# Kernel optimization log

Measured on AMD Instinct MI355X. Metric: run time of the kernel, lower is better.

## Reference

```python
import jax, jax.numpy as jnp
import numpy as np


def setup_inputs() -> dict:
    key = jax.random.key(0)
    k1, k2, k3 = jax.random.split(key, 3)
    B, C, D, S = 16, 80, 1024, 14  # batch, num_classes, feature dim, conv size
    return {
        "batch_size": B,
        "img_feature_map": jax.random.normal(k1, (B, D, S, S), dtype=jnp.float32),
        "word_features": jax.random.normal(k2, (C, D), dtype=jnp.float32),
        "fc_a_w": jax.random.normal(k3, (D,), dtype=jnp.float32) / np.float32(np.sqrt(D)),
        "fc_a_b": jnp.zeros((), dtype=jnp.float32),
    }


def reference(batch_size, img_feature_map, word_features, fc_a_w, fc_a_b):
    # img_feature_map: [B, D, H, W] -> [B, H, W, D]
    img = jnp.transpose(img_feature_map, (0, 2, 3, 1))
    # class-wise gated feature: tanh(img * word) -> [B, H, W, C, D]
    gated = jnp.tanh(img[:, :, :, None, :] * word_features[None, None, None, :, :])
    # rank-1 linear score: [B, H, W, C]
    scores = jnp.einsum('bhwcd,d->bhwc', gated, fc_a_w) + fc_a_b
    B, H, W, C = scores.shape
    # softmax over spatial positions (H*W) per (batch, class)
    coef = jax.nn.softmax(scores.reshape(B, H * W, C), axis=1).reshape(B, H, W, C)
    # attention-weighted spatial pooling -> [B, C, D]
    return jnp.einsum('bhwc,bhwd->bcd', coef, img)
```

## Files before the change

kernel.cpp:

```cpp
#include <hip/hip_runtime.h>

#define BB 16
#define CC 80
#define DD 1024
#define HW 196
#define NSP (BB * HW)
#define NCH 8
#define DCH 128
#define CPB 4
#define NCQ (CC / CPB)
#define PCL 16
#define TWO_LOG2E 2.8853900817779268f

__global__ __launch_bounds__(256) void scores_k(const float* __restrict__ img,
                                                const float* __restrict__ word,
                                                const float* __restrict__ fa,
                                                float* __restrict__ partial) {
    const int g = blockIdx.x * 256 + threadIdx.x;
    if (g >= NSP) return;
    const int b  = g / HW;
    const int hw = g - b * HW;
    const int d0 = blockIdx.y * DCH;
    const int c0 = blockIdx.z * CPB;

    const float* ip = img + ((size_t)b * DD + d0) * HW + hw;

    float p[CPB];
#pragma unroll
    for (int k = 0; k < CPB; ++k) p[k] = 0.f;

    for (int q = 0; q < DCH / 32; ++q) {
        float iv[32];
        const float* qp = ip + (size_t)q * 32 * HW;
#pragma unroll
        for (int i = 0; i < 32; ++i)
            iv[i] = qp[(size_t)i * HW] * TWO_LOG2E;

        const float* fp = fa + d0 + q * 32;
#pragma unroll
        for (int k = 0; k < CPB; ++k) {
            const float* wp = word + (size_t)(c0 + k) * DD + d0 + q * 32;
            float p0 = 0.f, p1 = 0.f;
#pragma unroll
            for (int i = 0; i < 32; i += 2) {
                float y0 = iv[i]     * wp[i];
                float y1 = iv[i + 1] * wp[i + 1];
                float e0 = __builtin_amdgcn_exp2f(y0);
                float e1 = __builtin_amdgcn_exp2f(y1);
                float r0 = __builtin_amdgcn_rcpf(e0 + 1.f);
                float r1 = __builtin_amdgcn_rcpf(e1 + 1.f);
                p0 = fmaf(fp[i],     r0, p0);
                p1 = fmaf(fp[i + 1], r1, p1);
            }
            p[k] += p0 + p1;
        }
    }

#pragma unroll
    for (int k = 0; k < CPB; ++k)
        partial[(((size_t)b * NCH + blockIdx.y) * CC + (c0 + k)) * HW + hw]
            = (-TWO_LOG2E) * p[k];
}

__global__ __launch_bounds__(256) void poolmax_k(const float* __restrict__ img,
                                                 const float* __restrict__ partial,
                                                 float* __restrict__ out) {
    __shared__ float it[64 * HW];
    __shared__ float ct[PCL * HW];
    const int b  = blockIdx.x;
    const int d0 = blockIdx.y * 64;
    const int cg = blockIdx.z * PCL;
    const int t  = threadIdx.x;
    const int w  = t >> 6, l = t & 63;

    const float4* src = (const float4*)(img + ((size_t)b * DD + d0) * HW);
    float4* dst = (float4*)it;
    for (int j = t; j < 64 * HW / 4; j += 256) dst[j] = src[j];

#pragma unroll
    for (int r = 4 * w; r < 4 * w + 4; ++r) {
        const int c = cg + r;
        float x0 = 0.f, x1 = 0.f, x2 = 0.f, x3 = 0.f;
#pragma unroll
        for (int ch = 0; ch < NCH; ++ch) {
            const float* pp = partial + (((size_t)b * NCH + ch) * CC + c) * HW;
            x0 += pp[l];
            x1 += pp[l + 64];
            x2 += pp[l + 128];
            if (l < HW - 192) x3 += pp[l + 192];
        }
        float x3m = (l < HW - 192) ? x3 : -3.4e38f;

        float m = fmaxf(fmaxf(x0, x1), fmaxf(x2, x3m));
#pragma unroll
        for (int off = 32; off >= 1; off >>= 1) m = fmaxf(m, __shfl_xor(m, off, 64));

        float e0 = __builtin_amdgcn_exp2f(x0 - m);
        float e1 = __builtin_amdgcn_exp2f(x1 - m);
        float e2 = __builtin_amdgcn_exp2f(x2 - m);
        float e3 = (l < HW - 192) ? __builtin_amdgcn_exp2f(x3 - m) : 0.f;

        float s = ((e0 + e1) + (e2 + e3));
#pragma unroll
        for (int off = 32; off >= 1; off >>= 1) s += __shfl_xor(s, off, 64);

        float inv = __builtin_amdgcn_rcpf(s);
        float* cr = ct + r * HW;
        cr[l]        = e0 * inv;
        cr[l + 64]   = e1 * inv;
        cr[l + 128]  = e2 * inv;
        if (l < HW - 192) cr[l + 192] = e3 * inv;
    }
    __syncthreads();

    const float* irow = it + l * HW;
    const float* crow = ct + (4 * w) * HW;

    float a0 = 0.f, a1 = 0.f, a2 = 0.f, a3 = 0.f;
    for (int h = 0; h < HW; h += 4) {
        float4 iv  = *(const float4*)(irow + h);
        float4 c0v = *(const float4*)(crow + h);
        float4 c1v = *(const float4*)(crow + HW + h);
        float4 c2v = *(const float4*)(crow + 2 * HW + h);
        float4 c3v = *(const float4*)(crow + 3 * HW + h);
        a0 = fmaf(iv.x, c0v.x, fmaf(iv.y, c0v.y, fmaf(iv.z, c0v.z, fmaf(iv.w, c0v.w, a0))));
        a1 = fmaf(iv.x, c1v.x, fmaf(iv.y, c1v.y, fmaf(iv.z, c1v.z, fmaf(iv.w, c1v.w, a1))));
        a2 = fmaf(iv.x, c2v.x, fmaf(iv.y, c2v.y, fmaf(iv.z, c2v.z, fmaf(iv.w, c2v.w, a2))));
        a3 = fmaf(iv.x, c3v.x, fmaf(iv.y, c3v.y, fmaf(iv.z, c3v.z, fmaf(iv.w, c3v.w, a3))));
    }

    float* op = out + ((size_t)b * CC + cg + 4 * w) * DD + d0 + l;
    op[0]          = a0;
    op[DD]         = a1;
    op[2 * (size_t)DD] = a2;
    op[3 * (size_t)DD] = a3;
}

extern "C" void kernel_launch(void* const* d_in, const int* in_sizes, int n_in,
                              void* d_out, int out_size, void* d_ws, size_t ws_size,
                              hipStream_t stream) {
    const float* img  = (const float*)d_in[1];
    const float* word = (const float*)d_in[2];
    const float* fa   = (const float*)d_in[3];
    float* out = (float*)d_out;

    float* partial = (float*)d_ws;

    scores_k<<<dim3((NSP + 255) / 256, NCH, NCQ), 256, 0, stream>>>(img, word, fa, partial);
    poolmax_k<<<dim3(BB, DD / 64, CC / PCL), 256, 0, stream>>>(img, partial, out);
}
```

Measured before the change: 181.6 us.

## Emit transposed image from scores kernel and pool directly from global memory

The scores kernel now also writes a [B, HW, D] transposed copy of the image feature map (only the blockIdx.z==0 slice does this). The pooling kernel then reads that copy from global memory with float4 loads along D, instead of staging a 64xHW image tile in LDS, and each thread accumulates 4 d-values across 4 classes. This removes the large LDS image tile, which should raise occupancy and give coalesced vector loads. In exchange it adds an extra full-image write in the scores kernel and needs a larger workspace.

After: 174.6 us. -3.8%, faster.

```diff
diff --git a/kernel.cpp b/kernel.cpp
--- a/kernel.cpp
+++ b/kernel.cpp
@@ -9,13 +9,14 @@
 #define DCH 128
 #define CPB 4
 #define NCQ (CC / CPB)
-#define PCL 16
+#define PTC 16
 #define TWO_LOG2E 2.8853900817779268f
 
 __global__ __launch_bounds__(256) void scores_k(const float* __restrict__ img,
                                                 const float* __restrict__ word,
                                                 const float* __restrict__ fa,
-                                                float* __restrict__ partial) {
+                                                float* __restrict__ partial,
+                                                float* __restrict__ imgT) {
     const int g = blockIdx.x * 256 + threadIdx.x;
     if (g >= NSP) return;
     const int b  = g / HW;
@@ -34,7 +35,18 @@
         const float* qp = ip + (size_t)q * 32 * HW;
 #pragma unroll
         for (int i = 0; i < 32; ++i)
-            iv[i] = qp[(size_t)i * HW] * TWO_LOG2E;
+            iv[i] = qp[(size_t)i * HW];
+
+        if (blockIdx.z == 0) {
+            float4* tp = (float4*)(imgT + (size_t)g * DD + d0 + q * 32);
+#pragma unroll
+            for (int i = 0; i < 8; ++i)
+                tp[i] = make_float4(iv[4 * i], iv[4 * i + 1], iv[4 * i + 2], iv[4 * i + 3]);
+        }
+
+#pragma unroll
+        for (int i = 0; i < 32; ++i)
+            iv[i] *= TWO_LOG2E;
 
         const float* fp = fa + d0 + q * 32;
 #pragma unroll
@@ -62,23 +74,19 @@
             = (-TWO_LOG2E) * p[k];
 }
 
-__global__ __launch_bounds__(256) void poolmax_k(const float* __restrict__ img,
-                                                 const float* __restrict__ partial,
-                                                 float* __restrict__ out) {
-    __shared__ float it[64 * HW];
-    __shared__ float ct[PCL * HW];
-    const int b  = blockIdx.x;
-    const int d0 = blockIdx.y * 64;
-    const int cg = blockIdx.z * PCL;
-    const int t  = threadIdx.x;
-    const int w  = t >> 6, l = t & 63;
-
-    const float4* src = (const float4*)(img + ((size_t)b * DD + d0) * HW);
-    float4* dst = (float4*)it;
-    for (int j = t; j < 64 * HW / 4; j += 256) dst[j] = src[j];
+__global__ __launch_bounds__(256) void poolT_k(const float* __restrict__ imgT,
+                                               const float* __restrict__ partial,
+                                               float* __restrict__ out) {
+    __shared__ float ct[PTC * HW];
+    const int b   = blockIdx.x;
+    const int dt0 = blockIdx.y * 256;
+    const int cg  = blockIdx.z * PTC;
+    const int t   = threadIdx.x;
+    const int w   = t >> 6, l = t & 63;
 
 #pragma unroll
-    for (int r = 4 * w; r < 4 * w + 4; ++r) {
+    for (int rr = 0; rr < 4; ++rr) {
+        const int r = 4 * w + rr;
         const int c = cg + r;
         float x0 = 0.f, x1 = 0.f, x2 = 0.f, x3 = 0.f;
 #pragma unroll
@@ -100,40 +108,49 @@
         float e2 = __builtin_amdgcn_exp2f(x2 - m);
         float e3 = (l < HW - 192) ? __builtin_amdgcn_exp2f(x3 - m) : 0.f;
 
-        float s = ((e0 + e1) + (e2 + e3));
+        float s = (e0 + e1) + (e2 + e3);
 #pragma unroll
         for (int off = 32; off >= 1; off >>= 1) s += __shfl_xor(s, off, 64);
 
         float inv = __builtin_amdgcn_rcpf(s);
         float* cr = ct + r * HW;
-        cr[l]        = e0 * inv;
-        cr[l + 64]   = e1 * inv;
-        cr[l + 128]  = e2 * inv;
+        cr[l]       = e0 * inv;
+        cr[l + 64]  = e1 * inv;
+        cr[l + 128] = e2 * inv;
         if (l < HW - 192) cr[l + 192] = e3 * inv;
     }
     __syncthreads();
 
-    const float* irow = it + l * HW;
     const float* crow = ct + (4 * w) * HW;
+    const float* ib = imgT + ((size_t)b * HW) * DD + dt0 + 4 * l;
 
-    float a0 = 0.f, a1 = 0.f, a2 = 0.f, a3 = 0.f;
+    float4 acc0 = {0,0,0,0}, acc1 = {0,0,0,0}, acc2 = {0,0,0,0}, acc3 = {0,0,0,0};
     for (int h = 0; h < HW; h += 4) {
-        float4 iv  = *(const float4*)(irow + h);
+        float4 i0 = *(const float4*)(ib + (size_t)(h    ) * DD);
+        float4 i1 = *(const float4*)(ib + (size_t)(h + 1) * DD);
+        float4 i2 = *(const float4*)(ib + (size_t)(h + 2) * DD);
+        float4 i3 = *(const float4*)(ib + (size_t)(h + 3) * DD);
         float4 c0v = *(const float4*)(crow + h);
         float4 c1v = *(const float4*)(crow + HW + h);
         float4 c2v = *(const float4*)(crow + 2 * HW + h);
         float4 c3v = *(const float4*)(crow + 3 * HW + h);
-        a0 = fmaf(iv.x, c0v.x, fmaf(iv.y, c0v.y, fmaf(iv.z, c0v.z, fmaf(iv.w, c0v.w, a0))));
-        a1 = fmaf(iv.x, c1v.x, fmaf(iv.y, c1v.y, fmaf(iv.z, c1v.z, fmaf(iv.w, c1v.w, a1))));
-        a2 = fmaf(iv.x, c2v.x, fmaf(iv.y, c2v.y, fmaf(iv.z, c2v.z, fmaf(iv.w, c2v.w, a2))));
-        a3 = fmaf(iv.x, c3v.x, fmaf(iv.y, c3v.y, fmaf(iv.z, c3v.z, fmaf(iv.w, c3v.w, a3))));
+#define ACC4(A, CV)                                                      \
+        A.x = fmaf(CV.x, i0.x, fmaf(CV.y, i1.x, fmaf(CV.z, i2.x, fmaf(CV.w, i3.x, A.x)))); \
+        A.y = fmaf(CV.x, i0.y, fmaf(CV.y, i1.y, fmaf(CV.z, i2.y, fmaf(CV.w, i3.y, A.y)))); \
+        A.z = fmaf(CV.x, i0.z, fmaf(CV.y, i1.z, fmaf(CV.z, i2.z, fmaf(CV.w, i3.z, A.z)))); \
+        A.w = fmaf(CV.x, i0.w, fmaf(CV.y, i1.w, fmaf(CV.z, i2.w, fmaf(CV.w, i3.w, A.w))));
+        ACC4(acc0, c0v)
+        ACC4(acc1, c1v)
+        ACC4(acc2, c2v)
+        ACC4(acc3, c3v)
+#undef ACC4
     }
 
-    float* op = out + ((size_t)b * CC + cg + 4 * w) * DD + d0 + l;
-    op[0]          = a0;
-    op[DD]         = a1;
-    op[2 * (size_t)DD] = a2;
-    op[3 * (size_t)DD] = a3;
+    float* ob = out + ((size_t)b * CC + cg + 4 * w) * DD + dt0 + 4 * l;
+    *(float4*)(ob)              = acc0;
+    *(float4*)(ob + DD)         = acc1;
+    *(float4*)(ob + 2 * (size_t)DD) = acc2;
+    *(float4*)(ob + 3 * (size_t)DD) = acc3;
 }
 
 extern "C" void kernel_launch(void* const* d_in, const int* in_sizes, int n_in,
@@ -145,7 +162,8 @@
     float* out = (float*)d_out;
 
     float* partial = (float*)d_ws;
+    float* imgT    = partial + (size_t)BB * NCH * CC * HW;
 
-    scores_k<<<dim3((NSP + 255) / 256, NCH, NCQ), 256, 0, stream>>>(img, word, fa, partial);
-    poolmax_k<<<dim3(BB, DD / 64, CC / PCL), 256, 0, stream>>>(img, partial, out);
+    scores_k<<<dim3((NSP + 255) / 256, NCH, NCQ), 256, 0, stream>>>(img, word, fa, partial, imgT);
+    poolT_k<<<dim3(BB, DD / 256, CC / PTC), 256, 0, stream>>>(imgT, partial, out);
 }
```
